# Performance work log

Measured on AMD Instinct MI355X. Metric: run time of the kernel, lower is better.

Reference implementation:

```python
import jax, jax.numpy as jnp
import numpy as np

B, S, D, H = 2, 2048, 2048, 16
HD = D // H          # 128 head dim
CAP = 50.0
FMIN = float(np.finfo(np.float32).min)
ROTARY_BASE = 10000.0


def setup_inputs() -> dict:
    key = jax.random.key(0)
    k0, k1, k2, k3, k4 = jax.random.split(key, 5)
    scale = 1.0 / np.sqrt(D)
    return {
        "hidden_states": jax.random.normal(k0, (B, S, D), dtype=jnp.float32),
        "wq": jax.random.normal(k1, (D, D), dtype=jnp.float32) * scale,
        "wk": jax.random.normal(k2, (D, D), dtype=jnp.float32) * scale,
        "wv": jax.random.normal(k3, (D, D), dtype=jnp.float32) * scale,
        "wo": jax.random.normal(k4, (D, D), dtype=jnp.float32) * scale,
    }


def _rotary_sincos(seq_len, dim):
    # fixed_pos_embedding_factory default branch (rotary_type='', scaling_factor=1)
    half = dim // 2
    fraction = 2.0 * jnp.arange(half, dtype=jnp.float32) / dim
    inv_freq = 1.0 / (ROTARY_BASE ** fraction)                 # [half]
    pos = jnp.arange(seq_len, dtype=jnp.float32)
    sinusoid = pos[:, None] * inv_freq[None, :]                # [S, half]
    return jnp.sin(sinusoid), jnp.cos(sinusoid)


def _apply_rotary(x, sin, cos):
    # x: [B, S, H, hd]; sin/cos: [S, hd//2] broadcast to [1, S, 1, hd//2]
    sin = sin[None, :, None, :]
    cos = cos[None, :, None, :]
    fh, sh = jnp.split(x, 2, axis=-1)
    return jnp.concatenate([fh * cos - sh * sin, sh * cos + fh * sin], axis=-1)


def _lingvo_softmax(x):
    # softmax with an extra zero logit in the denominator (use_extra_logit)
    max_logit = jnp.max(x, axis=-1, keepdims=True)
    max_logit = jnp.maximum(max_logit, 0.0)
    exp_x = jnp.exp(x - max_logit)
    denom = jnp.sum(exp_x, axis=-1, keepdims=True) + jnp.exp(-max_logit)
    return exp_x / denom


def reference(hidden_states, wq, wk, wv, wo):
    sin, cos = _rotary_sincos(S, HD)
    # projections (no bias); torch Linear y = x @ W^T -> here weights stored pre-transposed
    q = (hidden_states @ wq).reshape(B, S, H, HD)
    k = (hidden_states @ wk).reshape(B, S, H, HD)
    v = (hidden_states @ wv).reshape(B, S, H, HD)
    # rotary_pct = 1.0 -> rotate entire head dim
    q = _apply_rotary(q, sin, cos)
    k = _apply_rotary(k, sin, cos)
    # -> [B, H, S, hd], fp32 scores (module casts q,k to fp32)
    q = q.transpose(0, 2, 1, 3).astype(jnp.float32)
    k = k.transpose(0, 2, 1, 3).astype(jnp.float32)
    v = v.transpose(0, 2, 1, 3)
    # NOTE: no 1/sqrt(d) scaling, per original _attn
    attn = jnp.einsum('bhqd,bhkd->bhqk', q, k)
    causal = jnp.tril(jnp.ones((S, S), dtype=bool))[None, None]
    attn = jnp.where(causal, attn, FMIN)
    # logit cap (applied AFTER masking, as in original)
    attn = CAP * jnp.tanh(attn / CAP)
    probs = _lingvo_softmax(attn)
    out = jnp.einsum('bhqk,bhkd->bhqd', probs, v)
    out = out.transpose(0, 2, 1, 3).reshape(B, S, D)
    return out @ wo
```

## Files before the change

### kernel.cpp

```cpp
#include <hip/hip_runtime.h>

typedef _Float16 h16;
typedef __attribute__((ext_vector_type(8))) _Float16 half8;
typedef __attribute__((ext_vector_type(4))) float floatx4;

__device__ __forceinline__ h16 f2h(float f){ return (h16)f; }
__device__ __forceinline__ float h2f(h16 s){ return (float)s; }

#define GL2LDS(gp, lp) __builtin_amdgcn_global_load_lds( \
    (const __attribute__((address_space(1))) void*)(gp), \
    (__attribute__((address_space(3))) void*)(lp), 16, 0, 0)

__global__ __launch_bounds__(256) void hs_to_f16(const float* __restrict__ in,
                                                 h16* __restrict__ out, int n8){
  int i = blockIdx.x * 256 + threadIdx.x;
  if (i >= n8) return;
  floatx4 a = ((const floatx4*)in)[2*i];
  floatx4 b = ((const floatx4*)in)[2*i+1];
  half8 o;
  o[0]=f2h(a[0]); o[1]=f2h(a[1]); o[2]=f2h(a[2]); o[3]=f2h(a[3]);
  o[4]=f2h(b[0]); o[5]=f2h(b[1]); o[6]=f2h(b[2]); o[7]=f2h(b[3]);
  ((half8*)out)[i] = o;
}

__global__ __launch_bounds__(256) void wtrans(const float* __restrict__ wq,
                                              const float* __restrict__ wk,
                                              const float* __restrict__ wv,
                                              const float* __restrict__ wo,
                                              h16* __restrict__ wqkv_t,
                                              h16* __restrict__ wo_t){
  __shared__ float tile[32][33];
  int z = blockIdx.z;
  const float* src = (z==0)? wq : (z==1)? wk : (z==2)? wv : wo;
  h16* dst = (z<3) ? (wqkv_t + (size_t)z*2048*2048) : wo_t;
  int r0 = blockIdx.y*32, c0 = blockIdx.x*32;
  int t = threadIdx.x;
  int tr = t>>5, tc = t&31;
  for (int p=0;p<4;++p)
    tile[p*8+tr][tc] = src[(size_t)(r0+p*8+tr)*2048 + c0 + tc];
  __syncthreads();
  for (int p=0;p<4;++p)
    dst[(size_t)(c0+p*8+tr)*2048 + r0 + tc] = f2h(tile[tc][p*8+tr]);
}

template<bool OUT_F32>
__global__ __launch_bounds__(256) void gemm_bt(const h16* __restrict__ A,
                                               const h16* __restrict__ Bt,
                                               void* __restrict__ Cout,
                                               int M, int N, int K){
  __shared__ h16 a_lds[128*32];
  __shared__ h16 b_lds[128*32];
  const int t = threadIdx.x;
  const int m0 = blockIdx.y * 128, n0 = blockIdx.x * 128;
  const int wave = t >> 6, lane = t & 63, quad = lane >> 4, l16 = lane & 15;
  const int wm = (wave & 1) * 64, wn = (wave >> 1) * 64;
  const int srow = wave*16 + (lane >> 2);
  const int schunk = lane & 3;
  const h16* Abase = A  + (size_t)(m0 + srow)*K + schunk*8;
  const h16* Bbase = Bt + (size_t)(n0 + srow)*K + schunk*8;
  h16* aL = a_lds + wave*512;
  h16* bL = b_lds + wave*512;

  floatx4 zero4 = {0.f,0.f,0.f,0.f};
  floatx4 acc[4][4];
  for (int mi=0;mi<4;++mi) for (int ni=0;ni<4;++ni) acc[mi][ni] = zero4;

  for (int k0 = 0; k0 < K; k0 += 32){
    GL2LDS(Abase + k0,              aL);
    GL2LDS(Abase + (size_t)64*K+k0, aL + 2048);
    GL2LDS(Bbase + k0,              bL);
    GL2LDS(Bbase + (size_t)64*K+k0, bL + 2048);
    __syncthreads();
    half8 af[4], bfr[4];
    for (int mi=0;mi<4;++mi) af[mi]  = *(const half8*)(a_lds + (wm + mi*16 + l16)*32 + quad*8);
    for (int ni=0;ni<4;++ni) bfr[ni] = *(const half8*)(b_lds + (wn + ni*16 + l16)*32 + quad*8);
    for (int mi=0;mi<4;++mi)
      for (int ni=0;ni<4;++ni)
        acc[mi][ni] = __builtin_amdgcn_mfma_f32_16x16x32_f16(af[mi], bfr[ni], acc[mi][ni], 0,0,0);
    __syncthreads();
  }
  for (int mi=0;mi<4;++mi)
    for (int ni=0;ni<4;++ni)
      for (int r=0;r<4;++r){
        int row = m0 + wm + mi*16 + quad*4 + r;
        int col = n0 + wn + ni*16 + l16;
        float v = acc[mi][ni][r];
        if (OUT_F32) ((float*)Cout)[(size_t)row*N + col] = v;
        else         ((h16*)Cout)[(size_t)row*N + col] = f2h(v);
      }
}

__global__ __launch_bounds__(256) void rotary_split(const h16* __restrict__ qkv,
                                                    h16* __restrict__ qT,
                                                    h16* __restrict__ kT,
                                                    h16* __restrict__ vT){
  const int st = blockIdx.x, bh = blockIdx.y;
  const int b = bh >> 4, h = bh & 15;
  const int s0 = st * 64;
  const int t = threadIdx.x;
  for (int i = t; i < 4096; i += 256){
    int srow = i >> 6;
    int d = i & 63;
    int sg = s0 + srow;
    size_t m = (size_t)b*2048 + sg;
    size_t baseq = m*6144 + h*128;
    float inv = __expf(-0.14391157f * (float)d);
    float ang = (float)sg * inv;
    float sn, cs;
    __sincosf(ang, &sn, &cs);
    size_t dst = ((size_t)bh*2048 + sg)*128 + d;
    {
      float x1 = h2f(qkv[baseq + d]);
      float x2 = h2f(qkv[baseq + d + 64]);
      qT[dst]      = f2h(x1*cs - x2*sn);
      qT[dst + 64] = f2h(x2*cs + x1*sn);
    }
    {
      float x1 = h2f(qkv[baseq + 2048 + d]);
      float x2 = h2f(qkv[baseq + 2048 + d + 64]);
      kT[dst]      = f2h(x1*cs - x2*sn);
      kT[dst + 64] = f2h(x2*cs + x1*sn);
    }
  }
  for (int i = t; i < 8192; i += 256){
    int d = i >> 6, soff = i & 63;
    size_t m = (size_t)b*2048 + s0 + soff;
    h16 val = qkv[m*6144 + 4096 + h*128 + d];
    vT[((size_t)bh*128 + d)*2048 + s0 + soff] = val;
  }
}

__global__ __launch_bounds__(256) void flash_attn(const h16* __restrict__ qT,
                                                  const h16* __restrict__ kT,
                                                  const h16* __restrict__ vT,
                                                  h16* __restrict__ O){
  __shared__ h16 k_lds[64*136];
  __shared__ h16 v_lds[128*72];
  __shared__ h16 p_lds[4*16*72];
  const int t = threadIdx.x, wave = t>>6, lane = t&63, quad = lane>>4, l16 = lane&15;
  const int h = blockIdx.y, b = blockIdx.z;
  const int bh = b*16 + h;
  const int krow = t>>4, kch = t&15;
  const int vrow = t>>3, vch = t&7;
  const h16* kTb = kT + (size_t)bh*2048*128;
  const h16* vTb = vT + (size_t)bh*128*2048;
  floatx4 zero4 = {0.f,0.f,0.f,0.f};

  for (int half = 0; half < 2; ++half){
    const int qt = half ? 31 - (int)blockIdx.x : (int)blockIdx.x;
    const int q0 = qt*64;
    const size_t qrow = (size_t)bh*2048 + q0 + wave*16 + l16;
    half8 aq[4];
    for (int kc=0;kc<4;++kc) aq[kc] = *(const half8*)(qT + qrow*128 + kc*32 + quad*8);
    floatx4 acc_o[8];
    for (int nt=0;nt<8;++nt) acc_o[nt] = zero4;
    float mrow[4] = {0.f,0.f,0.f,0.f};
    float lrow[4] = {1.f,1.f,1.f,1.f};

    half8 kreg[4], vreg[4];
    for (int p=0;p<4;++p){
      kreg[p] = *(const half8*)(kTb + (size_t)(p*16 + krow)*128 + kch*8);
      vreg[p] = *(const half8*)(vTb + (size_t)(p*32 + vrow)*2048 + vch*8);
    }

    for (int kt = 0; kt <= qt; ++kt){
      const int kbase = kt*64;
      __syncthreads();
      for (int p=0;p<4;++p){
        *(half8*)(k_lds + (p*16 + krow)*136 + kch*8) = kreg[p];
        *(half8*)(v_lds + (p*32 + vrow)*72  + vch*8) = vreg[p];
      }
      __syncthreads();
      if (kt < qt){
        const int nb = kbase + 64;
        for (int p=0;p<4;++p){
          kreg[p] = *(const half8*)(kTb + (size_t)(nb + p*16 + krow)*128 + kch*8);
          vreg[p] = *(const half8*)(vTb + (size_t)(p*32 + vrow)*2048 + nb + vch*8);
        }
      }
      floatx4 s[4];
      for (int ni=0;ni<4;++ni){
        floatx4 a = zero4;
        for (int kc=0;kc<4;++kc){
          half8 bk = *(const half8*)(k_lds + (ni*16 + l16)*136 + kc*32 + quad*8);
          a = __builtin_amdgcn_mfma_f32_16x16x32_f16(aq[kc], bk, a, 0,0,0);
        }
        s[ni] = a;
      }
      float pm[4][4];
      float tmax[4] = {-1e30f,-1e30f,-1e30f,-1e30f};
      const bool diag = (kt == qt);
      for (int ni=0;ni<4;++ni){
        int col = kbase + ni*16 + l16;
        for (int r=0;r<4;++r){
          float e = __expf(s[ni][r] * 0.04f);
          float x = 50.f - 100.f * __builtin_amdgcn_rcpf(e + 1.f);
          if (diag){
            int row = q0 + wave*16 + quad*4 + r;
            if (col > row) x = -1e30f;
          }
          pm[ni][r] = x;
          tmax[r] = fmaxf(tmax[r], x);
        }
      }
      for (int r=0;r<4;++r)
        for (int off=1; off<16; off<<=1)
          tmax[r] = fmaxf(tmax[r], __shfl_xor(tmax[r], off, 16));
      float alpha[4], mnew[4], rsum[4];
      for (int r=0;r<4;++r){
        mnew[r] = fmaxf(mrow[r], tmax[r]);
        alpha[r] = __expf(mrow[r] - mnew[r]);
        mrow[r] = mnew[r];
        rsum[r] = 0.f;
      }
      for (int ni=0;ni<4;++ni)
        for (int r=0;r<4;++r){
          float p = __expf(pm[ni][r] - mnew[r]);
          pm[ni][r] = p;
          rsum[r] += p;
        }
      for (int r=0;r<4;++r){
        for (int off=1; off<16; off<<=1) rsum[r] += __shfl_xor(rsum[r], off, 16);
        lrow[r] = alpha[r]*lrow[r] + rsum[r];
      }
      for (int nt=0;nt<8;++nt)
        for (int r=0;r<4;++r) acc_o[nt][r] *= alpha[r];
      h16* pw = p_lds + wave*16*72;
      for (int ni=0;ni<4;++ni)
        for (int r=0;r<4;++r)
          pw[(quad*4+r)*72 + ni*16 + l16] = f2h(pm[ni][r]);
      __builtin_amdgcn_wave_barrier();
      half8 ap0 = *(const half8*)(pw + l16*72 + quad*8);
      half8 ap1 = *(const half8*)(pw + l16*72 + 32 + quad*8);
      for (int nt=0;nt<8;++nt){
        half8 bv0 = *(const half8*)(v_lds + (nt*16 + l16)*72 + quad*8);
        half8 bv1 = *(const half8*)(v_lds + (nt*16 + l16)*72 + 32 + quad*8);
        acc_o[nt] = __builtin_amdgcn_mfma_f32_16x16x32_f16(ap0, bv0, acc_o[nt], 0,0,0);
        acc_o[nt] = __builtin_amdgcn_mfma_f32_16x16x32_f16(ap1, bv1, acc_o[nt], 0,0,0);
      }
    }
    float invl[4];
    for (int r=0;r<4;++r) invl[r] = 1.0f / lrow[r];
    for (int nt=0;nt<8;++nt)
      for (int r=0;r<4;++r){
        int row = q0 + wave*16 + quad*4 + r;
        int col = h*128 + nt*16 + l16;
        O[((size_t)b*2048 + row)*2048 + col] = f2h(acc_o[nt][r] * invl[r]);
      }
  }
}

extern "C" void kernel_launch(void* const* d_in, const int* in_sizes, int n_in,
                              void* d_out, int out_size, void* d_ws, size_t ws_size,
                              hipStream_t stream){
  (void)in_sizes; (void)n_in; (void)out_size; (void)ws_size;
  const float* hs = (const float*)d_in[0];
  const float* wq = (const float*)d_in[1];
  const float* wk = (const float*)d_in[2];
  const float* wv = (const float*)d_in[3];
  const float* wo = (const float*)d_in[4];

  char* ws = (char*)d_ws;
  size_t off = 0;
  h16* hs_f   = (h16*)(ws + off); off += (size_t)4096*2048*2;
  h16* wqkv_t = (h16*)(ws + off); off += (size_t)6144*2048*2;
  h16* wo_t   = (h16*)(ws + off); off += (size_t)2048*2048*2;
  h16* qkv    = (h16*)(ws + off); off += (size_t)4096*6144*2;
  h16* qT     = (h16*)(ws + off); off += (size_t)4096*2048*2;
  h16* kT     = (h16*)(ws + off); off += (size_t)4096*2048*2;
  h16* vT     = (h16*)(ws + off); off += (size_t)4096*2048*2;
  h16* obuf   = qkv;

  hs_to_f16<<<dim3(4096), 256, 0, stream>>>(hs, hs_f, 4096*2048/8);
  wtrans<<<dim3(64,64,4), 256, 0, stream>>>(wq, wk, wv, wo, wqkv_t, wo_t);
  gemm_bt<false><<<dim3(48,32), 256, 0, stream>>>(hs_f, wqkv_t, (void*)qkv, 4096, 6144, 2048);
  rotary_split<<<dim3(32,32), 256, 0, stream>>>(qkv, qT, kT, vT);
  flash_attn<<<dim3(16,16,2), 256, 0, stream>>>(qT, kT, vT, obuf);
  gemm_bt<true><<<dim3(16,32), 256, 0, stream>>>(obuf, wo_t, d_out, 4096, 2048, 2048);
}
```

Before: 477.7 us.

## Fuse rotary embedding and head split into QKV GEMM epilogue

The QKV projection GEMM now stages its output tile in shared memory and writes rotated Q/K and transposed V directly into per-head layouts. This removes the separate rotary_split kernel and the full fp16 qkv intermediate buffer round-trip through global memory. Shared memory per block grows to hold the 128x130 output tile, which may lower occupancy, and the GEMM kernels are specialized to fixed sizes.

```diff
diff --git a/kernel.cpp b/kernel.cpp
--- a/kernel.cpp
+++ b/kernel.cpp
@@ -43,11 +43,83 @@
     dst[(size_t)(c0+p*8+tr)*2048 + r0 + tc] = f2h(tile[tc][p*8+tr]);
 }
 
-template<bool OUT_F32>
-__global__ __launch_bounds__(256) void gemm_bt(const h16* __restrict__ A,
-                                               const h16* __restrict__ Bt,
-                                               void* __restrict__ Cout,
-                                               int M, int N, int K){
+__global__ __launch_bounds__(256) void gemm_qkv(const h16* __restrict__ A,
+                                                const h16* __restrict__ Bt,
+                                                h16* __restrict__ qT,
+                                                h16* __restrict__ kT,
+                                                h16* __restrict__ vT){
+  const int K = 2048;
+  __shared__ h16 smem[128*130];
+  h16* a_lds = smem;
+  h16* b_lds = smem + 4096;
+  const int t = threadIdx.x;
+  const int m0 = blockIdx.y * 128, n0 = blockIdx.x * 128;
+  const int wave = t >> 6, lane = t & 63, quad = lane >> 4, l16 = lane & 15;
+  const int wm = (wave & 1) * 64, wn = (wave >> 1) * 64;
+  const int srow = wave*16 + (lane >> 2);
+  const int schunk = lane & 3;
+  const h16* Abase = A  + (size_t)(m0 + srow)*K + schunk*8;
+  const h16* Bbase = Bt + (size_t)(n0 + srow)*K + schunk*8;
+  h16* aL = a_lds + wave*512;
+  h16* bL = b_lds + wave*512;
+
+  floatx4 zero4 = {0.f,0.f,0.f,0.f};
+  floatx4 acc[4][4];
+  for (int mi=0;mi<4;++mi) for (int ni=0;ni<4;++ni) acc[mi][ni] = zero4;
+
+  for (int k0 = 0; k0 < K; k0 += 32){
+    GL2LDS(Abase + k0,              aL);
+    GL2LDS(Abase + (size_t)64*K+k0, aL + 2048);
+    GL2LDS(Bbase + k0,              bL);
+    GL2LDS(Bbase + (size_t)64*K+k0, bL + 2048);
+    __syncthreads();
+    half8 af[4], bfr[4];
+    for (int mi=0;mi<4;++mi) af[mi]  = *(const half8*)(a_lds + (wm + mi*16 + l16)*32 + quad*8);
+    for (int ni=0;ni<4;++ni) bfr[ni] = *(const half8*)(b_lds + (wn + ni*16 + l16)*32 + quad*8);
+    for (int mi=0;mi<4;++mi)
+      for (int ni=0;ni<4;++ni)
+        acc[mi][ni] = __builtin_amdgcn_mfma_f32_16x16x32_f16(af[mi], bfr[ni], acc[mi][ni], 0,0,0);
+    __syncthreads();
+  }
+  for (int mi=0;mi<4;++mi)
+    for (int ni=0;ni<4;++ni)
+      for (int r=0;r<4;++r)
+        smem[(wm + mi*16 + quad*4 + r)*130 + wn + ni*16 + l16] = f2h(acc[mi][ni][r]);
+  __syncthreads();
+  const int sec = n0 >> 11;
+  const int hh  = (n0 & 2047) >> 7;
+  const int bb  = m0 >> 11;
+  const int s0g = m0 & 2047;
+  const int bhg = bb*16 + hh;
+  if (sec < 2){
+    h16* dst = sec ? kT : qT;
+    const int d = t & 63;
+    const int g = t >> 6;
+    const float inv = __expf(-0.14391157f * (float)d);
+    for (int p=0;p<32;++p){
+      int sr = p*4 + g;
+      int s  = s0g + sr;
+      float sn, cs; __sincosf((float)s * inv, &sn, &cs);
+      float x1 = h2f(smem[sr*130 + d]);
+      float x2 = h2f(smem[sr*130 + d + 64]);
+      size_t o = ((size_t)bhg*2048 + s)*128 + d;
+      dst[o]      = f2h(x1*cs - x2*sn);
+      dst[o + 64] = f2h(x2*cs + x1*sn);
+    }
+  } else {
+    const int sr = t & 127;
+    const int g  = t >> 7;
+    for (int p=0;p<64;++p){
+      int d = p*2 + g;
+      vT[((size_t)bhg*128 + d)*2048 + s0g + sr] = smem[sr*130 + d];
+    }
+  }
+}
+
+__global__ __launch_bounds__(256) void gemm_out(const h16* __restrict__ A,
+                                                const h16* __restrict__ Bt,
+                                                float* __restrict__ Cout){
+  const int K = 2048, N = 2048;
   __shared__ h16 a_lds[128*32];
   __shared__ h16 b_lds[128*32];
   const int t = threadIdx.x;
@@ -84,50 +156,8 @@
       for (int r=0;r<4;++r){
         int row = m0 + wm + mi*16 + quad*4 + r;
         int col = n0 + wn + ni*16 + l16;
-        float v = acc[mi][ni][r];
-        if (OUT_F32) ((float*)Cout)[(size_t)row*N + col] = v;
-        else         ((h16*)Cout)[(size_t)row*N + col] = f2h(v);
-      }
-}
-
-__global__ __launch_bounds__(256) void rotary_split(const h16* __restrict__ qkv,
-                                                    h16* __restrict__ qT,
-                                                    h16* __restrict__ kT,
-                                                    h16* __restrict__ vT){
-  const int st = blockIdx.x, bh = blockIdx.y;
-  const int b = bh >> 4, h = bh & 15;
-  const int s0 = st * 64;
-  const int t = threadIdx.x;
-  for (int i = t; i < 4096; i += 256){
-    int srow = i >> 6;
-    int d = i & 63;
-    int sg = s0 + srow;
-    size_t m = (size_t)b*2048 + sg;
-    size_t baseq = m*6144 + h*128;
-    float inv = __expf(-0.14391157f * (float)d);
-    float ang = (float)sg * inv;
-    float sn, cs;
-    __sincosf(ang, &sn, &cs);
-    size_t dst = ((size_t)bh*2048 + sg)*128 + d;
-    {
-      float x1 = h2f(qkv[baseq + d]);
-      float x2 = h2f(qkv[baseq + d + 64]);
-      qT[dst]      = f2h(x1*cs - x2*sn);
-      qT[dst + 64] = f2h(x2*cs + x1*sn);
-    }
-    {
-      float x1 = h2f(qkv[baseq + 2048 + d]);
-      float x2 = h2f(qkv[baseq + 2048 + d + 64]);
-      kT[dst]      = f2h(x1*cs - x2*sn);
-      kT[dst + 64] = f2h(x2*cs + x1*sn);
-    }
-  }
-  for (int i = t; i < 8192; i += 256){
-    int d = i >> 6, soff = i & 63;
-    size_t m = (size_t)b*2048 + s0 + soff;
-    h16 val = qkv[m*6144 + 4096 + h*128 + d];
-    vT[((size_t)bh*128 + d)*2048 + s0 + soff] = val;
-  }
+        Cout[(size_t)row*N + col] = acc[mi][ni][r];
+      }
 }
 
 __global__ __launch_bounds__(256) void flash_attn(const h16* __restrict__ qT,
@@ -265,16 +295,14 @@
   h16* hs_f   = (h16*)(ws + off); off += (size_t)4096*2048*2;
   h16* wqkv_t = (h16*)(ws + off); off += (size_t)6144*2048*2;
   h16* wo_t   = (h16*)(ws + off); off += (size_t)2048*2048*2;
-  h16* qkv    = (h16*)(ws + off); off += (size_t)4096*6144*2;
   h16* qT     = (h16*)(ws + off); off += (size_t)4096*2048*2;
   h16* kT     = (h16*)(ws + off); off += (size_t)4096*2048*2;
   h16* vT     = (h16*)(ws + off); off += (size_t)4096*2048*2;
-  h16* obuf   = qkv;
+  h16* obuf   = (h16*)(ws + off); off += (size_t)4096*2048*2;
 
   hs_to_f16<<<dim3(4096), 256, 0, stream>>>(hs, hs_f, 4096*2048/8);
   wtrans<<<dim3(64,64,4), 256, 0, stream>>>(wq, wk, wv, wo, wqkv_t, wo_t);
-  gemm_bt<false><<<dim3(48,32), 256, 0, stream>>>(hs_f, wqkv_t, (void*)qkv, 4096, 6144, 2048);
-  rotary_split<<<dim3(32,32), 256, 0, stream>>>(qkv, qT, kT, vT);
+  gemm_qkv<<<dim3(48,32), 256, 0, stream>>>(hs_f, wqkv_t, qT, kT, vT);
   flash_attn<<<dim3(16,16,2), 256, 0, stream>>>(qT, kT, vT, obuf);
-  gemm_bt<true><<<dim3(16,32), 256, 0, stream>>>(obuf, wo_t, d_out, 4096, 2048, 2048);
-}
+  gemm_out<<<dim3(16,32), 256, 0, stream>>>(obuf, wo_t, (float*)d_out);
+}
```

Result: faster. 419.0 us (-12.3%).
